# Kernel tuning notes

Measured on AMD Instinct MI355X. Metric: run time of the kernel, lower is better.

## Reference

```python
import jax, jax.numpy as jnp
import numpy as np

# ProbLog program semantics, closed-form:
# Grid 2x2, cell index = 2*X + Y: 0=(0,0), 1=(0,1), 2=(1,0), 3=(1,1).
# Actions (query order): 0=stay, 1=up, 2=down, 3=left, 4=right.
# transition/5 only defines clauses for stay/up/down (plus west/east which never
# unify with left/right), so left/right can never produce 'unsafe'.
# unsafe :- pacman(X,Y), action(A), transition(X,Y,A,X1,Y1), ghost(X1,Y1).
# evidence(safe) conditions the action query: P(a|safe) = p_a(a)*safe(a)/sum.

def _build_T():
    T = np.zeros((5, 4, 4), dtype=np.float32)  # [action, pac_cell, ghost_cell]
    for c in range(4):
        T[0, c, c] = 1.0  # stay
    # up: (x,y)->(x,y+1): cell0->1, cell2->3 (y=1 cells move off-grid -> no ghost)
    T[1, 0, 1] = 1.0
    T[1, 2, 3] = 1.0
    # down: (x,y)->(x,y-1): cell1->0, cell3->2
    T[2, 1, 0] = 1.0
    T[2, 3, 2] = 1.0
    # left/right: no transition clauses -> always safe
    return T

_T = _build_T()


def setup_inputs() -> dict:
    key = jax.random.key(0)
    ks = jax.random.split(key, 4)
    B, H = 16384, 2048
    s = 1.0 / np.sqrt(H)
    return {
        "x": jax.random.normal(ks[0], (B, H), dtype=jnp.float32),
        "Wg": jax.random.normal(ks[1], (H, 4), dtype=jnp.float32) * s,
        "bg": jnp.zeros((4,), dtype=jnp.float32),
        "Wp": jax.random.normal(ks[2], (H, 4), dtype=jnp.float32) * s,
        "bp": jnp.zeros((4,), dtype=jnp.float32),
        "Wa": jax.random.normal(ks[3], (H, 5), dtype=jnp.float32) * s,
        "ba": jnp.zeros((5,), dtype=jnp.float32),
    }


def reference(x, Wg, bg, Wp, bp, Wa, ba):
    ghost = jax.nn.softmax(x @ Wg + bg, axis=-1)   # [B,4]
    pacman = jax.nn.softmax(x @ Wp + bp, axis=-1)  # [B,4]
    base = jax.nn.softmax(x @ Wa + ba, axis=-1)    # [B,5]
    T = jnp.asarray(_T)                            # [5,4,4]
    # P(unsafe | action=a) = sum_c pac[c] * ghost[target(c,a)]
    unsafe = jnp.einsum('bc,acd,bd->ba', pacman, T, ghost)  # [B,5]
    joint = base * (1.0 - unsafe)                  # P(action=a, safe)
    return joint / jnp.sum(joint, axis=-1, keepdims=True)   # P(action=a | safe)
```

## Files before the change

### kernel.cpp

```cpp
#include <hip/hip_runtime.h>


typedef __fp16 h2_t __attribute__((ext_vector_type(2)));
typedef __fp16 h4_t __attribute__((ext_vector_type(4)));

#define WS_PART_OFF 65536

__global__ void pack_weights(const float* __restrict__ Wg,
                             const float* __restrict__ Wp,
                             const float* __restrict__ Wa,
                             __fp16* __restrict__ wout)
{
    const int t = blockIdx.x * 256 + threadIdx.x;
    const int j = t >> 11, h = t & 2047;
    const int s = h >> 9, hk = h & 511;
    float v;
    if (j < 4)      v = Wg[h * 4 + j];
    else if (j < 8) v = Wp[h * 4 + (j - 4)];
    else            v = Wa[h * 5 + (j - 8)];
    wout[s * 6656 + j * 512 + hk] = (__fp16)v;
}

__global__ __launch_bounds__(256, 4)
void gemm_partial(const float* __restrict__ x,
                  const __fp16* __restrict__ wpk,
                  float* __restrict__ part)
{
    __shared__ __align__(16) __fp16 wl[13 * 512];

    const int tid = threadIdx.x;
    const int rt  = blockIdx.x & 511;
    const int s   = blockIdx.x >> 9;

    {
        const uint4* src = (const uint4*)(wpk + s * 6656);
        uint4* dst = (uint4*)wl;
        int i = tid;
        dst[i] = src[i]; i += 256;
        dst[i] = src[i]; i += 256;
        dst[i] = src[i]; i += 256;
        if (i < 832) dst[i] = src[i];
    }
    __syncthreads();

    const int w  = tid >> 6;
    const int l  = tid & 63;
    const int hs = l & 15;
    const int rg = l >> 4;
    const int row0 = rt * 32 + w * 8 + rg * 2;

    const float4* xg = (const float4*)x;
    const long b0 = (long)row0 * 512 + s * 128 + hs;
    const long b1 = b0 + 512;

    float4 xa[8], xb[8];
    #pragma unroll
    for (int c = 0; c < 8; ++c) {
        xa[c] = xg[b0 + c * 16];
        xb[c] = xg[b1 + c * 16];
    }

    float acc0[13], acc1[13];
    #pragma unroll
    for (int j = 0; j < 13; ++j) { acc0[j] = 0.f; acc1[j] = 0.f; }

    const h4_t* w4 = (const h4_t*)wl;

    #pragma unroll
    for (int c = 0; c < 8; ++c) {
        const h2_t xl0 = __builtin_amdgcn_cvt_pkrtz(xa[c].x, xa[c].y);
        const h2_t xh0 = __builtin_amdgcn_cvt_pkrtz(xa[c].z, xa[c].w);
        const h2_t xl1 = __builtin_amdgcn_cvt_pkrtz(xb[c].x, xb[c].y);
        const h2_t xh1 = __builtin_amdgcn_cvt_pkrtz(xb[c].z, xb[c].w);
        const int wb = c * 16 + hs;
        #pragma unroll
        for (int j = 0; j < 13; ++j) {
            const h4_t wv = w4[j * 128 + wb];
            const h2_t wlo = __builtin_shufflevector(wv, wv, 0, 1);
            const h2_t whi = __builtin_shufflevector(wv, wv, 2, 3);
#if __has_builtin(__builtin_amdgcn_fdot2)
            acc0[j] = __builtin_amdgcn_fdot2(xl0, wlo, acc0[j], false);
            acc0[j] = __builtin_amdgcn_fdot2(xh0, whi, acc0[j], false);
            acc1[j] = __builtin_amdgcn_fdot2(xl1, wlo, acc1[j], false);
            acc1[j] = __builtin_amdgcn_fdot2(xh1, whi, acc1[j], false);
#else
            acc0[j] += (float)xl0.x * (float)wlo.x + (float)xl0.y * (float)wlo.y
                     + (float)xh0.x * (float)whi.x + (float)xh0.y * (float)whi.y;
            acc1[j] += (float)xl1.x * (float)wlo.x + (float)xl1.y * (float)wlo.y
                     + (float)xh1.x * (float)whi.x + (float)xh1.y * (float)whi.y;
#endif
        }
    }

    #pragma unroll
    for (int j = 0; j < 13; ++j) {
        acc0[j] += __shfl_xor(acc0[j], 1, 64);
        acc0[j] += __shfl_xor(acc0[j], 2, 64);
        acc0[j] += __shfl_xor(acc0[j], 4, 64);
        acc0[j] += __shfl_xor(acc0[j], 8, 64);
        acc1[j] += __shfl_xor(acc1[j], 1, 64);
        acc1[j] += __shfl_xor(acc1[j], 2, 64);
        acc1[j] += __shfl_xor(acc1[j], 4, 64);
        acc1[j] += __shfl_xor(acc1[j], 8, 64);
    }

    float v0 = acc0[12], v1 = acc1[12];
    #pragma unroll
    for (int j = 11; j >= 0; --j) {
        v0 = (hs == j) ? acc0[j] : v0;
        v1 = (hs == j) ? acc1[j] : v1;
    }
    if (hs < 13) {
        const long pbase = ((long)(s << 14) + row0) * 13;
        part[pbase + hs]      = v0;
        part[pbase + 13 + hs] = v1;
    }
}

__global__ __launch_bounds__(256)
void reduce_epilogue(const float* __restrict__ part,
                     const float* __restrict__ bg, const float* __restrict__ bp,
                     const float* __restrict__ ba, float* __restrict__ out)
{
    const int r = blockIdx.x * 256 + threadIdx.x;

    float acc[13];
    #pragma unroll
    for (int j = 0; j < 13; ++j) acc[j] = 0.f;
    #pragma unroll
    for (int s = 0; s < 4; ++s) {
        const long pbase = ((long)(s << 14) + r) * 13;
        #pragma unroll
        for (int j = 0; j < 13; ++j) acc[j] += part[pbase + j];
    }

    const float g0 = acc[0] + bg[0], g1 = acc[1] + bg[1], g2 = acc[2] + bg[2], g3 = acc[3] + bg[3];
    const float q0 = acc[4] + bp[0], q1 = acc[5] + bp[1], q2 = acc[6] + bp[2], q3 = acc[7] + bp[3];
    const float a0 = acc[8] + ba[0], a1 = acc[9] + ba[1], a2 = acc[10] + ba[2],
                a3 = acc[11] + ba[3], a4 = acc[12] + ba[4];

    float m, sum, inv;
    m = fmaxf(fmaxf(g0, g1), fmaxf(g2, g3));
    const float eg0 = __expf(g0 - m), eg1 = __expf(g1 - m), eg2 = __expf(g2 - m), eg3 = __expf(g3 - m);
    sum = eg0 + eg1 + eg2 + eg3; inv = 1.f / sum;
    const float G0 = eg0 * inv, G1 = eg1 * inv, G2 = eg2 * inv, G3 = eg3 * inv;

    m = fmaxf(fmaxf(q0, q1), fmaxf(q2, q3));
    const float ep0 = __expf(q0 - m), ep1 = __expf(q1 - m), ep2 = __expf(q2 - m), ep3 = __expf(q3 - m);
    sum = ep0 + ep1 + ep2 + ep3; inv = 1.f / sum;
    const float P0 = ep0 * inv, P1 = ep1 * inv, P2 = ep2 * inv, P3 = ep3 * inv;

    m = fmaxf(fmaxf(fmaxf(a0, a1), fmaxf(a2, a3)), a4);
    const float ea0 = __expf(a0 - m), ea1 = __expf(a1 - m), ea2 = __expf(a2 - m),
                ea3 = __expf(a3 - m), ea4 = __expf(a4 - m);
    sum = ea0 + ea1 + ea2 + ea3 + ea4; inv = 1.f / sum;
    const float A0 = ea0 * inv, A1 = ea1 * inv, A2 = ea2 * inv, A3 = ea3 * inv, A4 = ea4 * inv;

    const float u0 = P0 * G0 + P1 * G1 + P2 * G2 + P3 * G3;
    const float u1 = P0 * G1 + P2 * G3;
    const float u2 = P1 * G0 + P3 * G2;

    const float j0 = A0 * (1.f - u0), j1 = A1 * (1.f - u1), j2 = A2 * (1.f - u2),
                j3 = A3, j4 = A4;
    const float isd = 1.f / (j0 + j1 + j2 + j3 + j4);

    float* o = out + (long)r * 5;
    o[0] = j0 * isd; o[1] = j1 * isd; o[2] = j2 * isd; o[3] = j3 * isd; o[4] = j4 * isd;
}

extern "C" void kernel_launch(void* const* d_in, const int* in_sizes, int n_in,
                              void* d_out, int out_size, void* d_ws, size_t ws_size,
                              hipStream_t stream) {
    const float* x  = (const float*)d_in[0];
    const float* Wg = (const float*)d_in[1];
    const float* bg = (const float*)d_in[2];
    const float* Wp = (const float*)d_in[3];
    const float* bp = (const float*)d_in[4];
    const float* Wa = (const float*)d_in[5];
    const float* ba = (const float*)d_in[6];
    float* out = (float*)d_out;

    __fp16* wpk = (__fp16*)d_ws;
    float* part = (float*)((char*)d_ws + WS_PART_OFF);

    pack_weights<<<104, 256, 0, stream>>>(Wg, Wp, Wa, wpk);
    gemm_partial<<<2048, 256, 0, stream>>>(x, wpk, part);
    reduce_epilogue<<<64, 256, 0, stream>>>(part, bg, bp, ba, out);
}
```

Before: 206.8 us.

## Halve rows per thread, double gemm grid, and issue x loads before LDS fill

Each thread now processes one row instead of two, so the gemm grid grows to 4096 blocks of 16 rows and register pressure drops. The global loads of x are moved ahead of the shared-memory weight fill and __syncthreads, so they can overlap the LDS copy. In exchange each block re-reads the weight slice from LDS for half as many rows, doubling the number of weight LDS reads per output row. The launch-bounds occupancy hint is also lowered from 4 to 3.

```diff
diff --git a/kernel.cpp b/kernel.cpp
--- a/kernel.cpp
+++ b/kernel.cpp
@@ -21,7 +21,7 @@
     wout[s * 6656 + j * 512 + hk] = (__fp16)v;
 }
 
-__global__ __launch_bounds__(256, 4)
+__global__ __launch_bounds__(256, 3)
 void gemm_partial(const float* __restrict__ x,
                   const __fp16* __restrict__ wpk,
                   float* __restrict__ part)
@@ -29,8 +29,21 @@
     __shared__ __align__(16) __fp16 wl[13 * 512];
 
     const int tid = threadIdx.x;
-    const int rt  = blockIdx.x & 511;
-    const int s   = blockIdx.x >> 9;
+    const int rt  = blockIdx.x & 1023;
+    const int s   = blockIdx.x >> 10;
+
+    const int w  = tid >> 6;
+    const int l  = tid & 63;
+    const int hs = l & 15;
+    const int rg = l >> 4;
+    const int row = rt * 16 + w * 4 + rg;
+
+    const float4* xg = (const float4*)x;
+    const long b0 = (long)row * 512 + s * 128 + hs;
+
+    float4 xa[8];
+    #pragma unroll
+    for (int c = 0; c < 8; ++c) xa[c] = xg[b0 + c * 16];
 
     {
         const uint4* src = (const uint4*)(wpk + s * 6656);
@@ -43,35 +56,16 @@
     }
     __syncthreads();
 
-    const int w  = tid >> 6;
-    const int l  = tid & 63;
-    const int hs = l & 15;
-    const int rg = l >> 4;
-    const int row0 = rt * 32 + w * 8 + rg * 2;
-
-    const float4* xg = (const float4*)x;
-    const long b0 = (long)row0 * 512 + s * 128 + hs;
-    const long b1 = b0 + 512;
-
-    float4 xa[8], xb[8];
+    float acc[13];
     #pragma unroll
-    for (int c = 0; c < 8; ++c) {
-        xa[c] = xg[b0 + c * 16];
-        xb[c] = xg[b1 + c * 16];
-    }
-
-    float acc0[13], acc1[13];
-    #pragma unroll
-    for (int j = 0; j < 13; ++j) { acc0[j] = 0.f; acc1[j] = 0.f; }
+    for (int j = 0; j < 13; ++j) acc[j] = 0.f;
 
     const h4_t* w4 = (const h4_t*)wl;
 
     #pragma unroll
     for (int c = 0; c < 8; ++c) {
-        const h2_t xl0 = __builtin_amdgcn_cvt_pkrtz(xa[c].x, xa[c].y);
-        const h2_t xh0 = __builtin_amdgcn_cvt_pkrtz(xa[c].z, xa[c].w);
-        const h2_t xl1 = __builtin_amdgcn_cvt_pkrtz(xb[c].x, xb[c].y);
-        const h2_t xh1 = __builtin_amdgcn_cvt_pkrtz(xb[c].z, xb[c].w);
+        const h2_t xl = __builtin_amdgcn_cvt_pkrtz(xa[c].x, xa[c].y);
+        const h2_t xh = __builtin_amdgcn_cvt_pkrtz(xa[c].z, xa[c].w);
         const int wb = c * 16 + hs;
         #pragma unroll
         for (int j = 0; j < 13; ++j) {
@@ -79,42 +73,28 @@
             const h2_t wlo = __builtin_shufflevector(wv, wv, 0, 1);
             const h2_t whi = __builtin_shufflevector(wv, wv, 2, 3);
 #if __has_builtin(__builtin_amdgcn_fdot2)
-            acc0[j] = __builtin_amdgcn_fdot2(xl0, wlo, acc0[j], false);
-            acc0[j] = __builtin_amdgcn_fdot2(xh0, whi, acc0[j], false);
-            acc1[j] = __builtin_amdgcn_fdot2(xl1, wlo, acc1[j], false);
-            acc1[j] = __builtin_amdgcn_fdot2(xh1, whi, acc1[j], false);
+            acc[j] = __builtin_amdgcn_fdot2(xl, wlo, acc[j], false);
+            acc[j] = __builtin_amdgcn_fdot2(xh, whi, acc[j], false);
 #else
-            acc0[j] += (float)xl0.x * (float)wlo.x + (float)xl0.y * (float)wlo.y
-                     + (float)xh0.x * (float)whi.x + (float)xh0.y * (float)whi.y;
-            acc1[j] += (float)xl1.x * (float)wlo.x + (float)xl1.y * (float)wlo.y
-                     + (float)xh1.x * (float)whi.x + (float)xh1.y * (float)whi.y;
+            acc[j] += (float)xl.x * (float)wlo.x + (float)xl.y * (float)wlo.y
+                    + (float)xh.x * (float)whi.x + (float)xh.y * (float)whi.y;
 #endif
         }
     }
 
     #pragma unroll
     for (int j = 0; j < 13; ++j) {
-        acc0[j] += __shfl_xor(acc0[j], 1, 64);
-        acc0[j] += __shfl_xor(acc0[j], 2, 64);
-        acc0[j] += __shfl_xor(acc0[j], 4, 64);
-        acc0[j] += __shfl_xor(acc0[j], 8, 64);
-        acc1[j] += __shfl_xor(acc1[j], 1, 64);
-        acc1[j] += __shfl_xor(acc1[j], 2, 64);
-        acc1[j] += __shfl_xor(acc1[j], 4, 64);
-        acc1[j] += __shfl_xor(acc1[j], 8, 64);
+        acc[j] += __shfl_xor(acc[j], 1, 64);
+        acc[j] += __shfl_xor(acc[j], 2, 64);
+        acc[j] += __shfl_xor(acc[j], 4, 64);
+        acc[j] += __shfl_xor(acc[j], 8, 64);
     }
 
-    float v0 = acc0[12], v1 = acc1[12];
+    float v = acc[12];
     #pragma unroll
-    for (int j = 11; j >= 0; --j) {
-        v0 = (hs == j) ? acc0[j] : v0;
-        v1 = (hs == j) ? acc1[j] : v1;
-    }
-    if (hs < 13) {
-        const long pbase = ((long)(s << 14) + row0) * 13;
-        part[pbase + hs]      = v0;
-        part[pbase + 13 + hs] = v1;
-    }
+    for (int j = 11; j >= 0; --j) v = (hs == j) ? acc[j] : v;
+    if (hs < 13)
+        part[((long)(s << 14) + row) * 13 + hs] = v;
 }
 
 __global__ __launch_bounds__(256)
@@ -184,6 +164,6 @@
     float* part = (float*)((char*)d_ws + WS_PART_OFF);
 
     pack_weights<<<104, 256, 0, stream>>>(Wg, Wp, Wa, wpk);
-    gemm_partial<<<2048, 256, 0, stream>>>(x, wpk, part);
+    gemm_partial<<<4096, 256, 0, stream>>>(x, wpk, part);
     reduce_epilogue<<<64, 256, 0, stream>>>(part, bg, bp, ba, out);
 }
```

New measurement: 208.9 us. Within noise of the previous version (+1.0%).
